# Optimization experiments

Measured on AMD Instinct MI355X. Metric: run time of the kernel, lower is better.

The kernel has to match this reference:

```python
import jax, jax.numpy as jnp
import numpy as np
import math

S_DIM = 512
Z_DIM = 64
B, L = 64, 512
NUM_HEADS = 4
HEAD_DIM = S_DIM // NUM_HEADS
N_AA = 20


def _layer_norm(x, eps=1e-5):
    mu = jnp.mean(x, axis=-1, keepdims=True)
    var = jnp.var(x, axis=-1, keepdims=True)
    return (x - mu) * jax.lax.rsqrt(var + eps)


def setup_inputs() -> dict:
    key = jax.random.key(0)
    ks = jax.random.split(key, 16)
    scale = 0.02
    d = {
        's': jax.random.normal(ks[0], (B, L, S_DIM), jnp.float32),
        'z': jax.random.normal(ks[1], (B, L, Z_DIM), jnp.float32),
        'wq': jax.random.normal(ks[2], (S_DIM, S_DIM), jnp.float32) * scale,
        'bq': jnp.zeros((S_DIM,), jnp.float32),
        'wk': jax.random.normal(ks[3], (S_DIM, S_DIM), jnp.float32) * scale,
        'bk': jnp.zeros((S_DIM,), jnp.float32),
        'wv': jax.random.normal(ks[4], (S_DIM, S_DIM), jnp.float32) * scale,
        'bv': jnp.zeros((S_DIM,), jnp.float32),
        'wo': jax.random.normal(ks[5], (S_DIM, S_DIM), jnp.float32) * scale,
        'bo': jnp.zeros((S_DIM,), jnp.float32),
        'wp': jax.random.normal(ks[6], (S_DIM, N_AA), jnp.float32) * scale,
        'bp': jnp.zeros((N_AA,), jnp.float32),
        'pos_bias': jax.random.normal(ks[7], (512,), jnp.float32) * 0.3,
        'entropy_weight': jnp.ones((1,), jnp.float32) * 0.1,
        'ln_g': jnp.ones((S_DIM,), jnp.float32),
        'ln_b': jnp.zeros((S_DIM,), jnp.float32),
        'w1': jax.random.normal(ks[8], (S_DIM, 4 * S_DIM), jnp.float32) * scale,
        'b1': jnp.zeros((4 * S_DIM,), jnp.float32),
        'w2': jax.random.normal(ks[9], (4 * S_DIM, S_DIM), jnp.float32) * scale,
        'b2': jnp.zeros((S_DIM,), jnp.float32),
    }
    return d


def reference(s, z, wq, bq, wk, bk, wv, bv, wo, bo, wp, bp, pos_bias,
              entropy_weight, ln_g, ln_b, w1, b1, w2, b2):
    Bc, Lc, D = s.shape
    H, hd = NUM_HEADS, D // NUM_HEADS

    s_ln = _layer_norm(s)  # non-affine F.layer_norm

    # sequence-profile entropy
    logits = s_ln @ wp + bp                      # [B,L,20]
    profile_probs = jax.nn.softmax(logits, axis=-1)
    position_entropy = -jnp.sum(profile_probs * jnp.log(profile_probs + 1e-8), axis=-1)  # [B,L]

    q = (s_ln @ wq + bq).reshape(Bc, Lc, H, hd)
    k = (s_ln @ wk + bk).reshape(Bc, Lc, H, hd)
    v = (s_ln @ wv + bv).reshape(Bc, Lc, H, hd)

    scores = jnp.einsum('blhd,bmhd->bhlm', q, k) / math.sqrt(hd)  # [B,H,L,L]

    # bias injected only at query index 0, using batch-0 entropy (as in torch code)
    entropy_guidance = -position_entropy[0, :Lc] * entropy_weight[0]  # [L]
    total_bias = entropy_guidance + pos_bias[:Lc]                      # [L]
    scores = scores.at[:, :, 0, :].add(total_bias[None, None, :])

    attn_weights = jax.nn.softmax(scores, axis=-1)                     # [B,H,L,L]
    attn_out = jnp.einsum('bhlm,bmhd->blhd', attn_weights, v).reshape(Bc, Lc, D)

    s2 = s + (attn_out @ wo + bo)

    h = _layer_norm(s2) * ln_g + ln_b
    ffn_out = jax.nn.relu(h @ w1 + b1) @ w2 + b2
    s3 = s2 + ffn_out

    return (s3, z, attn_weights[:, 0, :, :], position_entropy, profile_probs)
```

## Files before the change

kernel.cpp:

```cpp
#include <hip/hip_runtime.h>
#include <hip/hip_bf16.h>
#include <math.h>

#define SDIM 512
#define BATCH 64
#define LSEQ 512
#define NHEAD 4
#define HDIM 128
#define NAA 20
#define NROWS (BATCH * LSEQ)
#define LDQKV 1536

typedef __attribute__((ext_vector_type(8))) short short8;
typedef __attribute__((ext_vector_type(4))) float f32x4;

__device__ __forceinline__ unsigned short f2bf(float f) {
    unsigned int x = __float_as_uint(f);
    unsigned int r = (x + 0x7fffu + ((x >> 16) & 1u)) >> 16;
    return (unsigned short)r;
}
__device__ __forceinline__ float bf2f(unsigned short u) {
    return __uint_as_float((unsigned int)u << 16);
}

__device__ __forceinline__ void load16_lds(const void* g, void* lds) {
    __builtin_amdgcn_global_load_lds(
        (const __attribute__((address_space(1))) unsigned int*)g,
        (__attribute__((address_space(3))) unsigned int*)lds, 16, 0, 0);
}

__global__ __launch_bounds__(256) void wtrans(
    const float* __restrict__ W, unsigned short* __restrict__ Wt, int K, int N)
{
    __shared__ float tile[32][33];
    const int t = threadIdx.x, tx = t & 31, ty = t >> 5;
    const int n0 = blockIdx.x * 32, k0 = blockIdx.y * 32;
    #pragma unroll
    for (int p = 0; p < 4; p++)
        tile[ty + p * 8][tx] = W[(size_t)(k0 + ty + p * 8) * N + n0 + tx];
    __syncthreads();
    #pragma unroll
    for (int p = 0; p < 4; p++)
        Wt[(size_t)(n0 + ty + p * 8) * K + k0 + tx] = f2bf(tile[tx][ty + p * 8]);
}

__global__ __launch_bounds__(256) void wptrans(
    const float* __restrict__ wp, unsigned short* __restrict__ wpT)
{
    const int g = blockIdx.x * 256 + threadIdx.x;
    const int k = g & 511, j = g >> 9;
    float v = (j < NAA) ? wp[(size_t)k * NAA + j] : 0.0f;
    wpT[(size_t)j * 512 + k] = f2bf(v);
}

__global__ void bpack(const float* __restrict__ bq, const float* __restrict__ bk,
                      const float* __restrict__ bv, float* __restrict__ bqkv)
{
    int t = threadIdx.x;
    bqkv[t] = bq[t]; bqkv[512 + t] = bk[t]; bqkv[1024 + t] = bv[t];
}

template<int INMODE, bool AFFINE>
__global__ __launch_bounds__(256) void ln_kernel(
    const void* __restrict__ inp, unsigned short* __restrict__ out,
    const float* __restrict__ gamma, const float* __restrict__ beta)
{
    const int w = threadIdx.x >> 6, l = threadIdx.x & 63;
    const int r = blockIdx.x * 4 + w;

    float x[8];
    if (INMODE == 0) {
        const float* row = (const float*)inp + (size_t)r * SDIM;
        float4 a = *(const float4*)(row + l * 4);
        float4 b = *(const float4*)(row + 256 + l * 4);
        x[0] = a.x; x[1] = a.y; x[2] = a.z; x[3] = a.w;
        x[4] = b.x; x[5] = b.y; x[6] = b.z; x[7] = b.w;
    } else {
        const unsigned short* row = (const unsigned short*)inp + (size_t)r * SDIM;
        uint2 a = *(const uint2*)(row + l * 4);
        uint2 b = *(const uint2*)(row + 256 + l * 4);
        x[0] = bf2f((unsigned short)(a.x & 0xffff)); x[1] = bf2f((unsigned short)(a.x >> 16));
        x[2] = bf2f((unsigned short)(a.y & 0xffff)); x[3] = bf2f((unsigned short)(a.y >> 16));
        x[4] = bf2f((unsigned short)(b.x & 0xffff)); x[5] = bf2f((unsigned short)(b.x >> 16));
        x[6] = bf2f((unsigned short)(b.y & 0xffff)); x[7] = bf2f((unsigned short)(b.y >> 16));
    }

    float sum = 0.f, sq = 0.f;
    #pragma unroll
    for (int i = 0; i < 8; i++) { sum += x[i]; sq += x[i] * x[i]; }
    #pragma unroll
    for (int o = 1; o < 64; o <<= 1) {
        sum += __shfl_xor(sum, o);
        sq  += __shfl_xor(sq, o);
    }
    const float mean = sum * (1.0f / SDIM);
    const float var  = sq * (1.0f / SDIM) - mean * mean;
    const float inv  = rsqrtf(var + 1e-5f);

    float y[8];
    if (AFFINE) {
        float4 g0 = *(const float4*)(gamma + l * 4);
        float4 g1 = *(const float4*)(gamma + 256 + l * 4);
        float4 b0 = *(const float4*)(beta + l * 4);
        float4 b1 = *(const float4*)(beta + 256 + l * 4);
        y[0] = (x[0]-mean)*inv*g0.x + b0.x; y[1] = (x[1]-mean)*inv*g0.y + b0.y;
        y[2] = (x[2]-mean)*inv*g0.z + b0.z; y[3] = (x[3]-mean)*inv*g0.w + b0.w;
        y[4] = (x[4]-mean)*inv*g1.x + b1.x; y[5] = (x[5]-mean)*inv*g1.y + b1.y;
        y[6] = (x[6]-mean)*inv*g1.z + b1.z; y[7] = (x[7]-mean)*inv*g1.w + b1.w;
    } else {
        #pragma unroll
        for (int i = 0; i < 8; i++) y[i] = (x[i] - mean) * inv;
    }

    unsigned short* orow = out + (size_t)r * SDIM;
    uint2 p0, p1;
    p0.x = (unsigned)f2bf(y[0]) | ((unsigned)f2bf(y[1]) << 16);
    p0.y = (unsigned)f2bf(y[2]) | ((unsigned)f2bf(y[3]) << 16);
    p1.x = (unsigned)f2bf(y[4]) | ((unsigned)f2bf(y[5]) << 16);
    p1.y = (unsigned)f2bf(y[6]) | ((unsigned)f2bf(y[7]) << 16);
    *(uint2*)(orow + l * 4)       = p0;
    *(uint2*)(orow + 256 + l * 4) = p1;
}

__global__ __launch_bounds__(256) void profile_kernel(
    const unsigned short* __restrict__ A,
    const unsigned short* __restrict__ wpT,
    const float* __restrict__ bp,
    float* __restrict__ probs,
    float* __restrict__ pe)
{
    __shared__ __align__(16) unsigned short As[128 * 64];

    const int t = threadIdx.x;
    const int w = t >> 6, l = t & 63;
    const int lr = l & 15, lg = l >> 4;
    const int m0 = blockIdx.x * 128;

    f32x4 sacc[2][2];
    #pragma unroll
    for (int m = 0; m < 2; m++)
        #pragma unroll
        for (int n = 0; n < 2; n++)
            sacc[m][n] = (f32x4){0.f, 0.f, 0.f, 0.f};

    const int srow  = l >> 3;
    const int swz16 = ((l & 7) ^ srow) << 4;
    const char* pA[4];
    unsigned ldsoff[4];
    #pragma unroll
    for (int i = 0; i < 4; i++) {
        const int row = (w * 4 + i) * 8 + srow;
        pA[i] = (const char*)A + (size_t)(m0 + row) * 1024 + swz16;
        ldsoff[i] = (unsigned)(w * 4 + i) * 1024;
    }

    const int rsw   = (lr & 7) << 4;
    const int foff0 = (lg * 16) ^ rsw;
    const int foff1 = (64 + lg * 16) ^ rsw;
    int arow[2];
    #pragma unroll
    for (int m = 0; m < 2; m++) arow[m] = (w * 32 + m * 16 + lr) * 128;

    for (int k0 = 0; k0 < 512; k0 += 64) {
        const size_t kb = (size_t)k0 * 2;
        #pragma unroll
        for (int i = 0; i < 4; i++)
            load16_lds(pA[i] + kb, (char*)As + ldsoff[i]);
        __syncthreads();

        short8 af[2], bf[2];
        #pragma unroll
        for (int m = 0; m < 2; m++) af[m] = *(const short8*)((const char*)As + arow[m] + foff0);
        #pragma unroll
        for (int n = 0; n < 2; n++)
            bf[n] = *(const short8*)(wpT + (size_t)(n * 16 + lr) * 512 + k0 + lg * 8);
        #pragma unroll
        for (int m = 0; m < 2; m++)
            #pragma unroll
            for (int n = 0; n < 2; n++)
                sacc[m][n] = __builtin_amdgcn_mfma_f32_16x16x32_bf16(af[m], bf[n], sacc[m][n], 0, 0, 0);

        #pragma unroll
        for (int m = 0; m < 2; m++) af[m] = *(const short8*)((const char*)As + arow[m] + foff1);
        #pragma unroll
        for (int n = 0; n < 2; n++)
            bf[n] = *(const short8*)(wpT + (size_t)(n * 16 + lr) * 512 + k0 + 32 + lg * 8);
        #pragma unroll
        for (int m = 0; m < 2; m++)
            #pragma unroll
            for (int n = 0; n < 2; n++)
                sacc[m][n] = __builtin_amdgcn_mfma_f32_16x16x32_bf16(af[m], bf[n], sacc[m][n], 0, 0, 0);

        __syncthreads();
    }

    const float b0 = bp[lr];
    const float b1 = (lr < 4) ? bp[16 + lr] : 0.0f;
    #pragma unroll
    for (int m = 0; m < 2; m++) {
        #pragma unroll
        for (int j = 0; j < 4; j++) {
            const float v0 = sacc[m][0][j] + b0;
            const float e0 = __expf(v0);
            const float v1 = sacc[m][1][j] + b1;
            const float e1 = (lr < 4) ? __expf(v1) : 0.0f;
            float Sp = e0 + e1;
            float Tp = e0 * v0 + ((lr < 4) ? e1 * v1 : 0.0f);
            #pragma unroll
            for (int o = 1; o < 16; o <<= 1) {
                Sp += __shfl_xor(Sp, o);
                Tp += __shfl_xor(Tp, o);
            }
            const float inv = 1.0f / Sp;
            const int row = m0 + w * 32 + m * 16 + lg * 4 + j;
            probs[(size_t)row * NAA + lr] = e0 * inv;
            if (lr < 4) probs[(size_t)row * NAA + 16 + lr] = e1 * inv;
            if (lr == 0) pe[row] = logf(Sp) - Tp * inv;
        }
    }
}

__global__ void bias_kernel(const float* __restrict__ pe,
                            const float* __restrict__ ew,
                            const float* __restrict__ pos,
                            float* __restrict__ tb)
{
    int t = threadIdx.x;
    tb[t] = -pe[t] * ew[0] + pos[t];
}

template<int OMODE, bool BIAS, bool RELU, int RESID>
__global__ __launch_bounds__(512, 2) void mgemm7(
    const unsigned short* __restrict__ A, int lda,
    const unsigned short* __restrict__ Bt, int ldb,
    void* __restrict__ Cv, int ldc,
    const float* __restrict__ bias,
    const void* __restrict__ R, int ldr,
    int K)
{
    __shared__ __align__(16) char lds[131072];

    const int t = threadIdx.x;
    const int w = t >> 6, l = t & 63;
    const int wr = w >> 2, wc = w & 3;
    const int lg = l >> 4, lr = l & 15;

    const int gx   = gridDim.x;
    const int nwg  = gx * gridDim.y;
    const int flat = blockIdx.x + gx * blockIdx.y;
    const int cpx  = nwg >> 3;
    const int logical = (flat & 7) * cpx + (flat >> 3);
    const int m0 = (logical / gx) * 256, n0 = (logical % gx) * 256;

    f32x4 acc[8][4];
    #pragma unroll
    for (int m = 0; m < 8; m++)
        #pragma unroll
        for (int n = 0; n < 4; n++)
            acc[m][n] = (f32x4){0.f, 0.f, 0.f, 0.f};

    const int srow = t >> 3;
    const int sch  = (t & 7) ^ (srow & 7);

    auto stageA = [&](int kt, int d, int h) {
        const char* src = (const char*)A +
            ((size_t)(m0 + h * 128 + srow) * lda + sch * 8) * 2 + (size_t)kt * 128;
        char* dst = lds + d * 65536 + h * 16384 + t * 16;
        load16_lds(src, dst);
        load16_lds(src + (size_t)64 * lda * 2, dst + 8192);
    };
    auto stageB = [&](int kt, int d, int h) {
        const char* src = (const char*)Bt +
            ((size_t)(n0 + h * 128 + srow) * ldb + sch * 8) * 2 + (size_t)kt * 128;
        char* dst = lds + d * 65536 + 32768 + h * 16384 + t * 16;
        load16_lds(src, dst);
        load16_lds(src + (size_t)64 * ldb * 2, dst + 8192);
    };

    int aoff[4], boff[2], sw[2];
    #pragma unroll
    for (int mi = 0; mi < 4; mi++) aoff[mi] = (mi * 32 + wr * 16 + lr) * 128;
    #pragma unroll
    for (int ni = 0; ni < 2; ni++) boff[ni] = (ni * 64 + wc * 16 + lr) * 128;
    #pragma unroll
    for (int ks = 0; ks < 2; ks++) sw[ks] = ((ks * 4 + lg) ^ (lr & 7)) << 4;

    short8 afc[2][4];
    short8 bfc0[2][2];
    short8 bfc1[2][2];

    const int NI = K >> 7;

#define MPHASE(D, MH, NH, LOADA, LOADB, STAGE_STMT, WAIT_STMT) do {            \
    const char* Abase_ = lds + (D) * 65536 + (MH) * 16384;                     \
    const char* Bbase_ = lds + (D) * 65536 + 32768 + (NH) * 16384;             \
    if (LOADA) {                                                               \
        _Pragma("unroll")                                                      \
        for (int ks_ = 0; ks_ < 2; ks_++)                                      \
            _Pragma("unroll")                                                  \
            for (int mi_ = 0; mi_ < 4; mi_++)                                  \
                afc[ks_][mi_] = *(const short8*)(Abase_ + aoff[mi_] + sw[ks_]);\
    }                                                                          \
    short8 (&bf_)[2][2] = (NH) ? bfc1 : bfc0;                                  \
    if (LOADB) {                                                               \
        _Pragma("unroll")                                                      \
        for (int ks_ = 0; ks_ < 2; ks_++)                                      \
            _Pragma("unroll")                                                  \
            for (int ni_ = 0; ni_ < 2; ni_++)                                  \
                bf_[ks_][ni_] = *(const short8*)(Bbase_ + boff[ni_] + sw[ks_]);\
    }                                                                          \
    STAGE_STMT;                                                                \
    WAIT_STMT;                                                                 \
    __builtin_amdgcn_s_barrier();                                              \
    asm volatile("s_waitcnt lgkmcnt(0)" ::: "memory");                         \
    __builtin_amdgcn_sched_barrier(0);                                         \
    __builtin_amdgcn_s_setprio(1);                                             \
    _Pragma("unroll")                                                          \
    for (int ks_ = 0; ks_ < 2; ks_++)                                          \
        _Pragma("unroll")                                                      \
        for (int mi_ = 0; mi_ < 4; mi_++)                                      \
            _Pragma("unroll")                                                  \
            for (int ni_ = 0; ni_ < 2; ni_++)                                  \
                acc[(MH) * 4 + mi_][(NH) * 2 + ni_] =                          \
                    __builtin_amdgcn_mfma_f32_16x16x32_bf16(                   \
                        afc[ks_][mi_], bf_[ks_][ni_],                          \
                        acc[(MH) * 4 + mi_][(NH) * 2 + ni_], 0, 0, 0);         \
    __builtin_amdgcn_s_setprio(0);                                             \
    asm volatile("" ::: "memory");                                             \
    __builtin_amdgcn_s_barrier();                                              \
    asm volatile("" ::: "memory");                                             \
} while (0)

    stageA(0, 0, 0); stageB(0, 0, 0); stageB(0, 0, 1); stageA(0, 0, 1);
    stageA(1, 1, 0); stageB(1, 1, 0);
    asm volatile("s_waitcnt vmcnt(4)" ::: "memory");
    __builtin_amdgcn_s_barrier();
    asm volatile("" ::: "memory");

    for (int it = 0; it < NI; ++it) {
        const bool more = (it + 1 < NI);
        const int T1 = 2 * it + 1, T2 = 2 * it + 2, T3 = 2 * it + 3;

        MPHASE(0, 0, 0, 1, 1, { stageB(T1, 1, 1); }, {});
        MPHASE(0, 0, 1, 0, 1, { stageA(T1, 1, 1); }, {});
        MPHASE(0, 1, 0, 1, 0, { if (more) stageA(T2, 0, 0); }, {});
        MPHASE(0, 1, 1, 0, 0, { if (more) stageB(T2, 0, 0); },
               { if (more) { asm volatile("s_waitcnt vmcnt(4)" ::: "memory"); }
                 else      { asm volatile("s_waitcnt vmcnt(0)" ::: "memory"); } });
        MPHASE(1, 0, 0, 1, 1, { if (more) stageA(T2, 0, 1); }, {});
        MPHASE(1, 0, 1, 0, 1, { if (more) stageB(T2, 0, 1); }, {});
        MPHASE(1, 1, 0, 1, 0, { if (more) stageA(T3, 1, 0); }, {});
        MPHASE(1, 1, 1, 0, 0, { if (more) stageB(T3, 1, 0); },
               { if (more) { asm volatile("s_waitcnt vmcnt(4)" ::: "memory"); } });
    }
#undef MPHASE

    if (OMODE == 1) {
        unsigned short* cs = (unsigned short*)lds;
        #pragma unroll
        for (int nf = 0; nf < 4; nf++) {
            const int lcol = (nf >> 1) * 128 + (nf & 1) * 64 + wc * 16 + lr;
            const int col = n0 + lcol;
            const float bv = BIAS ? bias[col] : 0.0f;
            #pragma unroll
            for (int mf = 0; mf < 8; mf++) {
                const int lrow0 = (mf >> 2) * 128 + (mf & 3) * 32 + wr * 16 + lg * 4;
                #pragma unroll
                for (int j = 0; j < 4; j++) {
                    float v = acc[mf][nf][j] + bv;
                    if (RELU) v = fmaxf(v, 0.f);
                    const size_t grow = (size_t)(m0 + lrow0 + j);
                    if (RESID == 1) v += ((const float*)R)[grow * ldr + col];
                    if (RESID == 2) v += bf2f(((const unsigned short*)R)[grow * ldr + col]);
                    cs[(lrow0 + j) * 256 + lcol] = f2bf(v);
                }
            }
        }
        __syncthreads();
        unsigned short* Cp = (unsigned short*)Cv;
        #pragma unroll
        for (int i = 0; i < 16; i++) {
            const int slot = i * 512 + t;
            const int row = slot >> 5, c16 = slot & 31;
            short8 v = *(const short8*)(cs + row * 256 + c16 * 8);
            *(short8*)(Cp + (size_t)(m0 + row) * ldc + n0 + c16 * 8) = v;
        }
    } else {
        float* cf = (float*)lds;
        #pragma unroll
        for (int h = 0; h < 2; h++) {
            if (h) __syncthreads();
            #pragma unroll
            for (int nf = 0; nf < 4; nf++) {
                const int lcol = (nf >> 1) * 128 + (nf & 1) * 64 + wc * 16 + lr;
                const int col = n0 + lcol;
                const float bv = BIAS ? bias[col] : 0.0f;
                #pragma unroll
                for (int mi = 0; mi < 4; mi++) {
                    const int mf = h * 4 + mi;
                    const int lrow0 = (mf & 3) * 32 + wr * 16 + lg * 4;
                    #pragma unroll
                    for (int j = 0; j < 4; j++) {
                        float v = acc[mf][nf][j] + bv;
                        if (RELU) v = fmaxf(v, 0.f);
                        const size_t grow = (size_t)(m0 + h * 128 + lrow0 + j);
                        if (RESID == 1) v += ((const float*)R)[grow * ldr + col];
                        if (RESID == 2) v += bf2f(((const unsigned short*)R)[grow * ldr + col]);
                        cf[(lrow0 + j) * 256 + lcol] = v;
                    }
                }
            }
            __syncthreads();
            float* Cp = (float*)Cv;
            #pragma unroll
            for (int i = 0; i < 16; i++) {
                const int slot = i * 512 + t;
                const int row = slot >> 6, c4 = slot & 63;
                float4 v = *(const float4*)(cf + row * 256 + c4 * 4);
                *(float4*)(Cp + (size_t)(m0 + h * 128 + row) * ldc + n0 + c4 * 4) = v;
            }
        }
    }
}

__global__ __launch_bounds__(256, 3) void attn_mfma(
    const unsigned short* __restrict__ QKV,
    const float* __restrict__ tb,
    unsigned short* __restrict__ AOb,
    float* __restrict__ lgout)
{
    const int flat = blockIdx.x + 4 * (blockIdx.y + 4 * blockIdx.z);
    const int logical = ((flat & 7) << 7) + (flat >> 3);
    const int qt = logical & 3;
    const int h  = (logical >> 2) & 3;
    const int b  = logical >> 4;
    const int t  = threadIdx.x;
    const int w  = t >> 6, l = t & 63;
    const int lr = l & 15, lg = l >> 4;
    const int qbase = qt * 128 + w * 32;

    const unsigned short* Qp = QKV;
    const unsigned short* Kp = QKV + 512;
    const unsigned short* Vp = QKV + 1024;

    __shared__ __align__(16) unsigned short Ks[64 * 128];
    __shared__ __align__(16) unsigned short Vt[128 * 64];
    __shared__ __align__(16) unsigned short Pl[4 * 2048];
    __shared__ float tbs[512];

    tbs[t] = tb[t];
    tbs[t + 256] = tb[t + 256];

    short8 qf[2][4];
    #pragma unroll
    for (int fc = 0; fc < 2; fc++) {
        const size_t qrow = (size_t)(b * LSEQ + qbase + fc * 16 + lr) * LDQKV + h * HDIM;
        #pragma unroll
        for (int ks = 0; ks < 4; ks++)
            qf[fc][ks] = *(const short8*)(Qp + qrow + ks * 32 + lg * 8);
    }

    f32x4 oacc[2][8];
    #pragma unroll
    for (int m = 0; m < 2; m++)
        #pragma unroll
        for (int n = 0; n < 8; n++)
            oacc[m][n] = (f32x4){0.f, 0.f, 0.f, 0.f};
    float lpart[2] = {0.f, 0.f};

    const float scale = 0.08838834764831845f;
    unsigned short* Plw = Pl + w * 2048;

    for (int kt = 0; kt < 8; ++kt) {
        __syncthreads();

        const int k0 = (l & 31) * 2;
        const int d0 = w * 32 + (l >> 5) * 16;
        const size_t vrow = (size_t)(b * LSEQ + kt * 64 + k0) * LDQKV + h * HDIM + d0;
        short8 va0 = *(const short8*)(Vp + vrow);
        short8 va1 = *(const short8*)(Vp + vrow + 8);
        short8 vb0 = *(const short8*)(Vp + vrow + LDQKV);
        short8 vb1 = *(const short8*)(Vp + vrow + LDQKV + 8);

        #pragma unroll
        for (int it = 0; it < 4; it++) {
            const int bi = it * 4 + w;
            const int r  = bi * 4 + lg;
            const int sc = lr ^ (r & 7);
            const char* src = (const char*)Kp +
                (size_t)(b * LSEQ + kt * 64 + r) * (LDQKV * 2) + h * 256 + sc * 16;
            load16_lds(src, (char*)Ks + bi * 1024);
        }

        #pragma unroll
        for (int j = 0; j < 16; j++) {
            const int d = d0 + j;
            unsigned short lo = (unsigned short)((j < 8) ? va0[j] : va1[j - 8]);
            unsigned short hi = (unsigned short)((j < 8) ? vb0[j] : vb1[j - 8]);
            unsigned int pk = (unsigned)lo | ((unsigned)hi << 16);
            const int addr = d * 128 + ((((k0 >> 3) ^ (d & 7))) << 4) + (k0 & 7) * 2;
            *(unsigned int*)((char*)Vt + addr) = pk;
        }
        __syncthreads();

        f32x4 sacc[4][2];
        #pragma unroll
        for (int fm = 0; fm < 4; fm++)
            #pragma unroll
            for (int fc = 0; fc < 2; fc++)
                sacc[fm][fc] = (f32x4){0.f, 0.f, 0.f, 0.f};
        #pragma unroll
        for (int ks = 0; ks < 4; ks++) {
            short8 af[4];
            #pragma unroll
            for (int fm = 0; fm < 4; fm++) {
                const int r2 = fm * 16 + lr;
                af[fm] = *(const short8*)((const char*)Ks +
                          r2 * 256 + (((ks * 4 + lg) ^ (lr & 7)) << 4));
            }
            #pragma unroll
            for (int fm = 0; fm < 4; fm++)
                #pragma unroll
                for (int fc = 0; fc < 2; fc++)
                    sacc[fm][fc] = __builtin_amdgcn_mfma_f32_16x16x32_bf16(
                        af[fm], qf[fc][ks], sacc[fm][fc], 0, 0, 0);
        }

        #pragma unroll
        for (int fm = 0; fm < 4; fm++) {
            #pragma unroll
            for (int fc = 0; fc < 2; fc++) {
                float p0 = sacc[fm][fc][0] * scale;
                float p1 = sacc[fm][fc][1] * scale;
                float p2 = sacc[fm][fc][2] * scale;
                float p3 = sacc[fm][fc][3] * scale;
                if (qt == 0 && w == 0 && fc == 0 && lr == 0) {
                    const int kb = kt * 64 + fm * 16 + lg * 4;
                    p0 += tbs[kb + 0]; p1 += tbs[kb + 1];
                    p2 += tbs[kb + 2]; p3 += tbs[kb + 3];
                }
                p0 = __expf(p0); p1 = __expf(p1);
                p2 = __expf(p2); p3 = __expf(p3);
                lpart[fc] += (p0 + p1) + (p2 + p3);
                const int rq = fc * 16 + lr;
                const int chunk = fm * 2 + (lg >> 1);
                const int addr = rq * 128 + ((chunk ^ (rq & 7)) << 4) + (lg & 1) * 8;
                unsigned int lo = (unsigned)f2bf(p0) | ((unsigned)f2bf(p1) << 16);
                unsigned int hi = (unsigned)f2bf(p2) | ((unsigned)f2bf(p3) << 16);
                *(uint2*)((char*)Plw + addr) = make_uint2(lo, hi);
            }
        }

        #pragma unroll
        for (int ks2 = 0; ks2 < 2; ks2++) {
            short8 pf[2];
            #pragma unroll
            for (int fm2 = 0; fm2 < 2; fm2++) {
                const int rq2 = fm2 * 16 + lr;
                pf[fm2] = *(const short8*)((const char*)Plw +
                           rq2 * 128 + (((ks2 * 4 + lg) ^ (rq2 & 7)) << 4));
            }
            #pragma unroll
            for (int fn = 0; fn < 8; fn++) {
                const int d = fn * 16 + lr;
                short8 vf = *(const short8*)((const char*)Vt +
                             d * 128 + (((ks2 * 4 + lg) ^ (d & 7)) << 4));
                #pragma unroll
                for (int fm2 = 0; fm2 < 2; fm2++)
                    oacc[fm2][fn] = __builtin_amdgcn_mfma_f32_16x16x32_bf16(
                        pf[fm2], vf, oacc[fm2][fn], 0, 0, 0);
            }
        }
    }

    float l0 = lpart[0], l1 = lpart[1];
    l0 += __shfl_xor(l0, 16); l0 += __shfl_xor(l0, 32);
    l1 += __shfl_xor(l1, 16); l1 += __shfl_xor(l1, 32);
    float* lw = (float*)Plw;
    if (lg == 0) { lw[lr] = l0; lw[16 + lr] = l1; }
    if (h == 0 && lg == 0) {
        lgout[b * LSEQ + qbase + lr]      = l0;
        lgout[b * LSEQ + qbase + 16 + lr] = l1;
    }
    __builtin_amdgcn_s_waitcnt(0);

    #pragma unroll
    for (int fm2 = 0; fm2 < 2; fm2++) {
        float linv[4];
        #pragma unroll
        for (int j = 0; j < 4; j++)
            linv[j] = 1.0f / lw[fm2 * 16 + lg * 4 + j];
        #pragma unroll
        for (int fn = 0; fn < 8; fn++) {
            const int d = fn * 16 + lr;
            #pragma unroll
            for (int j = 0; j < 4; j++) {
                const int q = qbase + fm2 * 16 + lg * 4 + j;
                AOb[(size_t)(b * LSEQ + q) * SDIM + h * HDIM + d] =
                    f2bf(oacc[fm2][fn][j] * linv[j]);
            }
        }
    }
}

__global__ __launch_bounds__(256) void sw0_kernel(
    const unsigned short* __restrict__ QKV,
    const float* __restrict__ tb,
    const float* __restrict__ lsum,
    float* __restrict__ W0)
{
    const int flat = blockIdx.x + 4 * blockIdx.y;
    const int logical = ((flat & 7) << 5) + (flat >> 3);
    const int qt = logical & 3;
    const int b  = logical >> 2;
    const int t  = threadIdx.x;
    const int w  = t >> 6, l = t & 63;
    const int lr = l & 15, lg = l >> 4;
    const int qbase = qt * 128 + w * 32;

    const unsigned short* Qp = QKV;
    const unsigned short* Kp = QKV + 512;

    __shared__ __align__(16) unsigned short Ks[64 * 128];
    __shared__ __align__(16) float Sc[4][32][68];

    short8 qf[2][4];
    #pragma unroll
    for (int fc = 0; fc < 2; fc++) {
        const size_t qrow = (size_t)(b * LSEQ + qbase + fc * 16 + lr) * LDQKV;
        #pragma unroll
        for (int ks = 0; ks < 4; ks++)
            qf[fc][ks] = *(const short8*)(Qp + qrow + ks * 32 + lg * 8);
    }

    float linv[2];
    linv[0] = 1.0f / lsum[b * LSEQ + qbase + lr];
    linv[1] = 1.0f / lsum[b * LSEQ + qbase + 16 + lr];

    const float scale = 0.08838834764831845f;

    for (int kt = 0; kt < 8; ++kt) {
        __syncthreads();
        #pragma unroll
        for (int it = 0; it < 4; it++) {
            const int bi = it * 4 + w;
            const int r  = bi * 4 + lg;
            const int sc = lr ^ (r & 7);
            const char* src = (const char*)Kp +
                (size_t)(b * LSEQ + kt * 64 + r) * (LDQKV * 2) + sc * 16;
            load16_lds(src, (char*)Ks + bi * 1024);
        }
        __syncthreads();

        f32x4 sacc[4][2];
        #pragma unroll
        for (int fm = 0; fm < 4; fm++)
            #pragma unroll
            for (int fc = 0; fc < 2; fc++)
                sacc[fm][fc] = (f32x4){0.f, 0.f, 0.f, 0.f};
        #pragma unroll
        for (int ks = 0; ks < 4; ks++) {
            short8 af[4];
            #pragma unroll
            for (int fm = 0; fm < 4; fm++) {
                const int r2 = fm * 16 + lr;
                af[fm] = *(const short8*)((const char*)Ks +
                          r2 * 256 + (((ks * 4 + lg) ^ (lr & 7)) << 4));
            }
            #pragma unroll
            for (int fm = 0; fm < 4; fm++)
                #pragma unroll
                for (int fc = 0; fc < 2; fc++)
                    sacc[fm][fc] = __builtin_amdgcn_mfma_f32_16x16x32_bf16(
                        af[fm], qf[fc][ks], sacc[fm][fc], 0, 0, 0);
        }

        #pragma unroll
        for (int fm = 0; fm < 4; fm++) {
            #pragma unroll
            for (int fc = 0; fc < 2; fc++) {
                float p0 = sacc[fm][fc][0] * scale;
                float p1 = sacc[fm][fc][1] * scale;
                float p2 = sacc[fm][fc][2] * scale;
                float p3 = sacc[fm][fc][3] * scale;
                if (qt == 0 && w == 0 && fc == 0 && lr == 0) {
                    const int kb = kt * 64 + fm * 16 + lg * 4;
                    p0 += tb[kb + 0]; p1 += tb[kb + 1];
                    p2 += tb[kb + 2]; p3 += tb[kb + 3];
                }
                p0 = __expf(p0) * linv[fc]; p1 = __expf(p1) * linv[fc];
                p2 = __expf(p2) * linv[fc]; p3 = __expf(p3) * linv[fc];
                *(float4*)&Sc[w][fc * 16 + lr][fm * 16 + lg * 4] =
                    make_float4(p0, p1, p2, p3);
            }
        }

        #pragma unroll
        for (int i = 0; i < 8; i++) {
            const int row = i * 4 + lg;
            float4 v = *(const float4*)&Sc[w][row][lr * 4];
            *(float4*)(W0 + (size_t)(b * LSEQ + qbase + row) * LSEQ +
                       kt * 64 + lr * 4) = v;
        }
    }
}

extern "C" void kernel_launch(void* const* d_in, const int* in_sizes, int n_in,
                              void* d_out, int out_size, void* d_ws, size_t ws_size,
                              hipStream_t stream)
{
    const float* s   = (const float*)d_in[0];
    const float* z   = (const float*)d_in[1];
    const float* wq  = (const float*)d_in[2];
    const float* bq  = (const float*)d_in[3];
    const float* wk  = (const float*)d_in[4];
    const float* bk  = (const float*)d_in[5];
    const float* wv  = (const float*)d_in[6];
    const float* bv  = (const float*)d_in[7];
    const float* wo  = (const float*)d_in[8];
    const float* bo  = (const float*)d_in[9];
    const float* wp  = (const float*)d_in[10];
    const float* bp  = (const float*)d_in[11];
    const float* pos = (const float*)d_in[12];
    const float* ew  = (const float*)d_in[13];
    const float* lng = (const float*)d_in[14];
    const float* lnb = (const float*)d_in[15];
    const float* w1  = (const float*)d_in[16];
    const float* b1  = (const float*)d_in[17];
    const float* w2  = (const float*)d_in[18];
    const float* b2  = (const float*)d_in[19];

    float* out = (float*)d_out;
    const size_t oz  = (size_t)NROWS * SDIM;
    const size_t ow  = oz + (size_t)NROWS * 64;
    const size_t ope = ow + (size_t)NROWS * LSEQ;
    const size_t opr = ope + (size_t)NROWS;

    char* wsb = (char*)d_ws;
    unsigned short* QKV = (unsigned short*)(wsb);
    unsigned short* F   = (unsigned short*)(wsb);
    unsigned short* Xb  = (unsigned short*)(wsb + 100663296);
    unsigned short* s2b = (unsigned short*)(wsb + 134217728);
    unsigned short* hb  = (unsigned short*)(wsb + 167772160);
    unsigned short* wqkvt = (unsigned short*)(wsb + 234881024);
    unsigned short* wot = wqkvt + 786432;
    unsigned short* w1t = wqkvt + 1048576;
    unsigned short* w2t = wqkvt + 2097152;
    unsigned short* wpT = wqkvt + 3145728;
    float* bqkv = (float*)(wsb + 234881024 + 6324224);
    float* tb   = bqkv + 1536;
    float* lgv  = tb + 512;

    wtrans<<<dim3(16, 16), 256, 0, stream>>>(wq, wqkvt, 512, 512);
    wtrans<<<dim3(16, 16), 256, 0, stream>>>(wk, wqkvt + 262144, 512, 512);
    wtrans<<<dim3(16, 16), 256, 0, stream>>>(wv, wqkvt + 524288, 512, 512);
    wtrans<<<dim3(16, 16), 256, 0, stream>>>(wo, wot, 512, 512);
    wtrans<<<dim3(64, 16), 256, 0, stream>>>(w1, w1t, 512, 2048);
    wtrans<<<dim3(16, 64), 256, 0, stream>>>(w2, w2t, 2048, 512);
    wptrans<<<64, 256, 0, stream>>>(wp, wpT);
    bpack<<<1, 512, 0, stream>>>(bq, bk, bv, bqkv);

    ln_kernel<0, false><<<NROWS / 4, 256, 0, stream>>>(s, Xb, nullptr, nullptr);

    profile_kernel<<<256, 256, 0, stream>>>(Xb, wpT, bp, out + opr, out + ope);

    bias_kernel<<<1, 512, 0, stream>>>(out + ope, ew, pos, tb);

    mgemm7<1, true, false, 0><<<dim3(6, 128), 512, 0, stream>>>(
        Xb, 512, wqkvt, 512, QKV, LDQKV, bqkv, nullptr, 0, 512);

    attn_mfma<<<dim3(4, NHEAD, BATCH), 256, 0, stream>>>(
        QKV, tb, Xb, lgv);

    sw0_kernel<<<dim3(4, BATCH), 256, 0, stream>>>(QKV, tb, lgv, out + ow);

    mgemm7<1, true, false, 1><<<dim3(2, 128), 512, 0, stream>>>(
        Xb, 512, wot, 512, s2b, 512, bo, s, 512, 512);

    ln_kernel<1, true><<<NROWS / 4, 256, 0, stream>>>(s2b, hb, lng, lnb);

    mgemm7<1, true, true, 0><<<dim3(8, 128), 512, 0, stream>>>(
        hb, 512, w1t, 512, F, 2048, b1, nullptr, 0, 512);

    mgemm7<0, true, false, 2><<<dim3(2, 128), 512, 0, stream>>>(
        F, 2048, w2t, 2048, out, 512, b2, s2b, 512, 2048);

    hipMemcpyAsync(out + oz, z, (size_t)NROWS * 64 * sizeof(float),
                   hipMemcpyDeviceToDevice, stream);
}
```

Measured before the change: 454.8 us.

## Double-buffer K tiles and prefetch V registers in attention kernel

```diff
diff --git a/kernel.cpp b/kernel.cpp
--- a/kernel.cpp
+++ b/kernel.cpp
@@ -423,7 +423,7 @@
     }
 }
 
-__global__ __launch_bounds__(256, 3) void attn_mfma(
+__global__ __launch_bounds__(256, 2) void attn_mfma(
     const unsigned short* __restrict__ QKV,
     const float* __restrict__ tb,
     unsigned short* __restrict__ AOb,
@@ -443,9 +443,9 @@
     const unsigned short* Kp = QKV + 512;
     const unsigned short* Vp = QKV + 1024;
 
-    __shared__ __align__(16) unsigned short Ks[64 * 128];
-    __shared__ __align__(16) unsigned short Vt[128 * 64];
-    __shared__ __align__(16) unsigned short Pl[4 * 2048];
+    __shared__ __align__(16) unsigned short Ks[2][8192];
+    __shared__ __align__(16) unsigned short Vt[8192];
+    __shared__ __align__(16) unsigned short Pl[8192];
     __shared__ float tbs[512];
 
     tbs[t] = tb[t];
@@ -471,17 +471,7 @@
     const float scale = 0.08838834764831845f;
     unsigned short* Plw = Pl + w * 2048;
 
-    for (int kt = 0; kt < 8; ++kt) {
-        __syncthreads();
-
-        const int k0 = (l & 31) * 2;
-        const int d0 = w * 32 + (l >> 5) * 16;
-        const size_t vrow = (size_t)(b * LSEQ + kt * 64 + k0) * LDQKV + h * HDIM + d0;
-        short8 va0 = *(const short8*)(Vp + vrow);
-        short8 va1 = *(const short8*)(Vp + vrow + 8);
-        short8 vb0 = *(const short8*)(Vp + vrow + LDQKV);
-        short8 vb1 = *(const short8*)(Vp + vrow + LDQKV + 8);
-
+    auto stageK = [&](int kt, int buf) {
         #pragma unroll
         for (int it = 0; it < 4; it++) {
             const int bi = it * 4 + w;
@@ -489,19 +479,55 @@
             const int sc = lr ^ (r & 7);
             const char* src = (const char*)Kp +
                 (size_t)(b * LSEQ + kt * 64 + r) * (LDQKV * 2) + h * 256 + sc * 16;
-            load16_lds(src, (char*)Ks + bi * 1024);
-        }
+            load16_lds(src, (char*)Ks[buf] + bi * 1024);
+        }
+    };
+    const int k0v = (l & 31) * 2;
+    const int d0v = w * 32 + (l >> 5) * 16;
+
+    stageK(0, 0);
+    short8 vc0, vc1, vc2, vc3, vn0, vn1, vn2, vn3;
+    {
+        const size_t vrow = (size_t)(b * LSEQ + k0v) * LDQKV + h * HDIM + d0v;
+        vc0 = *(const short8*)(Vp + vrow);
+        vc1 = *(const short8*)(Vp + vrow + 8);
+        vc2 = *(const short8*)(Vp + vrow + LDQKV);
+        vc3 = *(const short8*)(Vp + vrow + LDQKV + 8);
+    }
+
+    #pragma unroll 2
+    for (int kt = 0; kt < 8; ++kt) {
+        asm volatile("" ::: "memory");
+        __builtin_amdgcn_s_barrier();
+        asm volatile("" ::: "memory");
+
+        if (kt < 7) {
+            stageK(kt + 1, (kt + 1) & 1);
+            const size_t vrow = (size_t)(b * LSEQ + (kt + 1) * 64 + k0v) * LDQKV + h * HDIM + d0v;
+            vn0 = *(const short8*)(Vp + vrow);
+            vn1 = *(const short8*)(Vp + vrow + 8);
+            vn2 = *(const short8*)(Vp + vrow + LDQKV);
+            vn3 = *(const short8*)(Vp + vrow + LDQKV + 8);
+        }
+        asm volatile("" ::: "memory");
 
         #pragma unroll
         for (int j = 0; j < 16; j++) {
-            const int d = d0 + j;
-            unsigned short lo = (unsigned short)((j < 8) ? va0[j] : va1[j - 8]);
-            unsigned short hi = (unsigned short)((j < 8) ? vb0[j] : vb1[j - 8]);
+            const int d = d0v + j;
+            unsigned short lo = (unsigned short)((j < 8) ? vc0[j] : vc1[j - 8]);
+            unsigned short hi = (unsigned short)((j < 8) ? vc2[j] : vc3[j - 8]);
             unsigned int pk = (unsigned)lo | ((unsigned)hi << 16);
-            const int addr = d * 128 + ((((k0 >> 3) ^ (d & 7))) << 4) + (k0 & 7) * 2;
+            const int addr = d * 128 + ((((k0v >> 3) ^ (d & 7))) << 4) + (k0v & 7) * 2;
             *(unsigned int*)((char*)Vt + addr) = pk;
         }
-        __syncthreads();
+
+        if (kt < 7) { asm volatile("s_waitcnt vmcnt(8)" ::: "memory"); }
+        else        { asm volatile("s_waitcnt vmcnt(0)" ::: "memory"); }
+        asm volatile("s_waitcnt lgkmcnt(0)" ::: "memory");
+        __builtin_amdgcn_s_barrier();
+        __builtin_amdgcn_sched_barrier(0);
+
+        const unsigned short* Ksb = Ks[kt & 1];
 
         f32x4 sacc[4][2];
         #pragma unroll
@@ -515,7 +541,7 @@
             #pragma unroll
             for (int fm = 0; fm < 4; fm++) {
                 const int r2 = fm * 16 + lr;
-                af[fm] = *(const short8*)((const char*)Ks +
+                af[fm] = *(const short8*)((const char*)Ksb +
                           r2 * 256 + (((ks * 4 + lg) ^ (lr & 7)) << 4));
             }
             #pragma unroll
@@ -571,6 +597,8 @@
                         pf[fm2], vf, oacc[fm2][fn], 0, 0, 0);
             }
         }
+
+        vc0 = vn0; vc1 = vn1; vc2 = vn2; vc3 = vn3;
     }
 
     float l0 = lpart[0], l1 = lpart[1];
```

Measured after the change: 424.1 us. 1.07x faster.
